# Performance work log

Measured on AMD Instinct MI355X. Metric: run time of the kernel, lower is better.

Reference implementation:

```python
import jax, jax.numpy as jnp
import numpy as np

SCALE = 0.08838834764831845  # 1/sqrt(128)


def setup_inputs() -> dict:
    key = jax.random.key(0)
    k1, k2, k3, k4 = jax.random.split(key, 4)
    B, Hq, Hkv, D = 32, 32, 8, 128
    block_size, max_blocks = 16, 256
    num_blocks = B * max_blocks  # 8192; identity paging layout
    q = jax.random.normal(k1, (B, 1, Hq, D), dtype=jnp.float32)
    k_cache = jax.random.normal(k2, (num_blocks, block_size, Hkv, D), dtype=jnp.float32)
    v_cache = jax.random.normal(k3, (num_blocks, block_size, Hkv, D), dtype=jnp.float32)
    cache_seqlens = jax.random.randint(k4, (B,), 1, block_size * max_blocks + 1, dtype=jnp.int32)
    block_table = jnp.arange(B * max_blocks, dtype=jnp.int32).reshape(B, max_blocks)
    return {"q": q, "k_cache": k_cache, "v_cache": v_cache,
            "cache_seqlens": cache_seqlens, "block_table": block_table}


def reference(q, k_cache, v_cache, cache_seqlens, block_table):
    # Decode-time paged attention (flash_attn_with_kvcache path).
    B, _, Hq, D = q.shape
    block_size, Hkv = k_cache.shape[1], k_cache.shape[2]
    G = Hq // Hkv  # GQA group size
    # Block-table gather: [B, max_blocks, bs, Hkv, D] -> [B, T, Hkv, D]
    k = k_cache[block_table].reshape(B, -1, Hkv, D)
    v = v_cache[block_table].reshape(B, -1, Hkv, D)
    T = k.shape[1]
    # GQA without materializing repeated KV heads: fold q heads into [Hkv, G]
    qg = q[:, 0].reshape(B, Hkv, G, D)
    scores = jnp.einsum('bkgd,btkd->bkgt', qg, k) * SCALE  # [B, Hkv, G, T]
    valid = jnp.arange(T, dtype=jnp.int32)[None, :] < cache_seqlens[:, None]  # [B, T]
    scores = jnp.where(valid[:, None, None, :], scores, -jnp.inf)
    probs = jax.nn.softmax(scores.astype(jnp.float32), axis=-1).astype(q.dtype)
    out = jnp.einsum('bkgt,btkd->bkgd', probs, v)  # [B, Hkv, G, D]
    return out.reshape(B, Hq, D)
```

## Files before the change

### kernel.cpp

```cpp
#include <hip/hip_runtime.h>
#include <math.h>


#define NUM_B    32
#define HQ       32
#define HKV      8
#define GG       4
#define DD       128
#define PAGE     16
#define MAXPAGES 256
#define SPLITS   16
#define CHUNK    256

static constexpr float SCALE_F = 0.08838834764831845f;
static constexpr float NEG     = -1e30f;

static __device__ __forceinline__ float dot8(const float4& qa, const float4& qb,
                                             const float4& ka, const float4& kb) {
    return qa.x * ka.x + qa.y * ka.y + qa.z * ka.z + qa.w * ka.w +
           qb.x * kb.x + qb.y * kb.y + qb.z * kb.z + qb.w * kb.w;
}

__global__ __launch_bounds__(64) void attn_split_kernel(
    const float* __restrict__ q,
    const float* __restrict__ kc,
    const float* __restrict__ vc,
    const int*   __restrict__ seqlens,
    const int*   __restrict__ btab,
    float*       __restrict__ accW,
    float*       __restrict__ mlW)
{
    const int bid   = blockIdx.x;
    const int split = bid & (SPLITS - 1);
    const int kvh   = (bid >> 4) & (HKV - 1);
    const int b     = bid >> 7;
    const int lane  = threadIdx.x;
    const int tg    = lane >> 4;
    const int ds    = lane & 15;

    const long pbase   = ((long)(b * HKV + kvh) * SPLITS + split) * GG;
    const long accBase = pbase * DD;
    const long mlBase  = pbase * 2;

    const int T  = seqlens[b];
    const int t0 = split * CHUNK;

    if (t0 >= T) {
        if (tg == 0) {
            const float4 z = make_float4(0.f, 0.f, 0.f, 0.f);
            #pragma unroll
            for (int g = 0; g < GG; ++g) {
                *(float4*)(accW + accBase + g * DD + ds * 8)     = z;
                *(float4*)(accW + accBase + g * DD + ds * 8 + 4) = z;
            }
            if (ds == 0) {
                #pragma unroll
                for (int g = 0; g < GG; ++g) {
                    mlW[mlBase + g * 2]     = NEG;
                    mlW[mlBase + g * 2 + 1] = 0.f;
                }
            }
        }
        return;
    }

    const int t1 = min(T, t0 + CHUNK);

    float4 q0[GG], q1[GG];
    #pragma unroll
    for (int g = 0; g < GG; ++g) {
        const float* qp = q + (long)(b * HQ + kvh * GG + g) * DD + ds * 8;
        q0[g] = *(const float4*)qp;
        q1[g] = *(const float4*)(qp + 4);
    }

    float m[GG], l[GG], acc[GG][8];
    #pragma unroll
    for (int g = 0; g < GG; ++g) {
        m[g] = NEG;
        l[g] = 0.f;
        #pragma unroll
        for (int j = 0; j < 8; ++j) acc[g][j] = 0.f;
    }

    const int btab_b = b * MAXPAGES;
    auto load_kv = [&](int tb, float4& k0, float4& k1, float4& v0, float4& v1) {
        const int t = min(tb + tg, t1 - 1);
        const int page = btab[btab_b + (t >> 4)];
        const long off = (((long)page * PAGE + (t & 15)) * HKV + kvh) * DD + ds * 8;
        k0 = *(const float4*)(kc + off);
        k1 = *(const float4*)(kc + off + 4);
        v0 = *(const float4*)(vc + off);
        v1 = *(const float4*)(vc + off + 4);
    };

    float4 k0, k1, v0, v1;
    load_kv(t0, k0, k1, v0, v1);

    for (int tb = t0; tb < t1; tb += 4) {
        const bool valid = (tb + tg) < t1;
        const float4 ck0 = k0, ck1 = k1, cv0 = v0, cv1 = v1;
        load_kv(tb + 4, k0, k1, v0, v1);

        #pragma unroll
        for (int g = 0; g < GG; ++g) {
            float s = dot8(q0[g], q1[g], ck0, ck1);
            s += __shfl_xor(s, 1);
            s += __shfl_xor(s, 2);
            s += __shfl_xor(s, 4);
            s += __shfl_xor(s, 8);
            s = valid ? s * SCALE_F : NEG;
            const float mn    = fmaxf(m[g], s);
            const float alpha = __expf(m[g] - mn);
            const float p     = valid ? __expf(s - mn) : 0.f;
            l[g] = l[g] * alpha + p;
            m[g] = mn;
            acc[g][0] = acc[g][0] * alpha + p * cv0.x;
            acc[g][1] = acc[g][1] * alpha + p * cv0.y;
            acc[g][2] = acc[g][2] * alpha + p * cv0.z;
            acc[g][3] = acc[g][3] * alpha + p * cv0.w;
            acc[g][4] = acc[g][4] * alpha + p * cv1.x;
            acc[g][5] = acc[g][5] * alpha + p * cv1.y;
            acc[g][6] = acc[g][6] * alpha + p * cv1.z;
            acc[g][7] = acc[g][7] * alpha + p * cv1.w;
        }
    }

    #pragma unroll
    for (int g = 0; g < GG; ++g) {
        float M2 = m[g];
        M2 = fmaxf(M2, __shfl_xor(M2, 16));
        M2 = fmaxf(M2, __shfl_xor(M2, 32));
        const float alpha = __expf(m[g] - M2);
        float lg = l[g] * alpha;
        lg += __shfl_xor(lg, 16);
        lg += __shfl_xor(lg, 32);
        float a[8];
        #pragma unroll
        for (int j = 0; j < 8; ++j) {
            float x = acc[g][j] * alpha;
            x += __shfl_xor(x, 16);
            x += __shfl_xor(x, 32);
            a[j] = x;
        }
        if (tg == 0) {
            const float4 o0 = make_float4(a[0], a[1], a[2], a[3]);
            const float4 o1 = make_float4(a[4], a[5], a[6], a[7]);
            *(float4*)(accW + accBase + g * DD + ds * 8)     = o0;
            *(float4*)(accW + accBase + g * DD + ds * 8 + 4) = o1;
            if (ds == 0) {
                mlW[mlBase + g * 2]     = M2;
                mlW[mlBase + g * 2 + 1] = lg;
            }
        }
    }
}

__global__ __launch_bounds__(128) void attn_reduce_kernel(
    const float* __restrict__ accW,
    const float* __restrict__ mlW,
    float*       __restrict__ out)
{
    const int bid = blockIdx.x;
    const int g   = bid & 3;
    const int kvh = (bid >> 2) & 7;
    const int b   = bid >> 5;
    const int d   = threadIdx.x;

    const long base = (long)(b * HKV + kvh) * SPLITS * GG;

    float ms[SPLITS], ls[SPLITS];
    float M = NEG;
    #pragma unroll
    for (int s = 0; s < SPLITS; ++s) {
        ms[s] = mlW[(base + s * GG + g) * 2];
        ls[s] = mlW[(base + s * GG + g) * 2 + 1];
        M = fmaxf(M, ms[s]);
    }
    float L = 0.f, o = 0.f;
    #pragma unroll
    for (int s = 0; s < SPLITS; ++s) {
        const float w = __expf(ms[s] - M);
        L += ls[s] * w;
        o += w * accW[(base + s * GG + g) * DD + d];
    }
    out[(long)(b * HQ + kvh * GG + g) * DD + d] = o / L;
}

extern "C" void kernel_launch(void* const* d_in, const int* in_sizes, int n_in,
                              void* d_out, int out_size, void* d_ws, size_t ws_size,
                              hipStream_t stream)
{
    const float* q       = (const float*)d_in[0];
    const float* kc      = (const float*)d_in[1];
    const float* vc      = (const float*)d_in[2];
    const int*   seqlens = (const int*)d_in[3];
    const int*   btab    = (const int*)d_in[4];
    float*       out     = (float*)d_out;

    float* accW = (float*)d_ws;
    float* mlW  = accW + (size_t)NUM_B * HKV * SPLITS * GG * DD;

    attn_split_kernel<<<NUM_B * HKV * SPLITS, 64, 0, stream>>>(
        q, kc, vc, seqlens, btab, accW, mlW);
    attn_reduce_kernel<<<NUM_B * HKV * GG, DD, 0, stream>>>(accW, mlW, out);
}
```

Baseline: 913.8 us.

## Double KV splits, prefetch two steps ahead, and cache page indices in registers

Raises the split count from 16 to 32 with 128-token chunks, which doubles the number of workgroups and gives more parallel memory streams. The loop now keeps two K/V loads in flight instead of one. Each lane preloads one page-table entry, and pages are fetched with a cross-lane shuffle instead of a global btab read every step. Empty splits now write only the max and sum values and skip zeroing the accumulator; the reduce weights those slots by exp(-huge)=0, so a NaN or Inf left in the uninitialised workspace could still leak into the output.

```diff
diff --git a/kernel.cpp b/kernel.cpp
--- a/kernel.cpp
+++ b/kernel.cpp
@@ -9,8 +9,8 @@
 #define DD       128
 #define PAGE     16
 #define MAXPAGES 256
-#define SPLITS   16
-#define CHUNK    256
+#define SPLITS   32
+#define CHUNK    128
 
 static constexpr float SCALE_F = 0.08838834764831845f;
 static constexpr float NEG     = -1e30f;
@@ -32,8 +32,8 @@
 {
     const int bid   = blockIdx.x;
     const int split = bid & (SPLITS - 1);
-    const int kvh   = (bid >> 4) & (HKV - 1);
-    const int b     = bid >> 7;
+    const int kvh   = (bid / SPLITS) & (HKV - 1);
+    const int b     = bid / (SPLITS * HKV);
     const int lane  = threadIdx.x;
     const int tg    = lane >> 4;
     const int ds    = lane & 15;
@@ -46,25 +46,19 @@
     const int t0 = split * CHUNK;
 
     if (t0 >= T) {
-        if (tg == 0) {
-            const float4 z = make_float4(0.f, 0.f, 0.f, 0.f);
-            #pragma unroll
-            for (int g = 0; g < GG; ++g) {
-                *(float4*)(accW + accBase + g * DD + ds * 8)     = z;
-                *(float4*)(accW + accBase + g * DD + ds * 8 + 4) = z;
-            }
-            if (ds == 0) {
-                #pragma unroll
-                for (int g = 0; g < GG; ++g) {
-                    mlW[mlBase + g * 2]     = NEG;
-                    mlW[mlBase + g * 2 + 1] = 0.f;
-                }
-            }
+        if (lane < GG) {
+            mlW[mlBase + lane * 2]     = NEG;
+            mlW[mlBase + lane * 2 + 1] = 0.f;
         }
         return;
     }
 
-    const int t1 = min(T, t0 + CHUNK);
+    const int t1    = min(T, t0 + CHUNK);
+    const int iters = (t1 - t0 + 3) >> 2;
+
+    const int lastp    = (T - 1) >> 4;
+    const int pidx     = min((t0 >> 4) + (lane & 15), lastp);
+    const int page_reg = btab[b * MAXPAGES + pidx];
 
     float4 q0[GG], q1[GG];
     #pragma unroll
@@ -83,10 +77,11 @@
         for (int j = 0; j < 8; ++j) acc[g][j] = 0.f;
     }
 
-    const int btab_b = b * MAXPAGES;
-    auto load_kv = [&](int tb, float4& k0, float4& k1, float4& v0, float4& v1) {
-        const int t = min(tb + tg, t1 - 1);
-        const int page = btab[btab_b + (t >> 4)];
+    auto load_iter = [&](int j, float4& k0, float4& k1, float4& v0, float4& v1) {
+        j = min(j, iters - 1);
+        const int tb   = t0 + 4 * j;
+        const int t    = min(tb + tg, t1 - 1);
+        const int page = __shfl(page_reg, (tb - t0) >> 4);
         const long off = (((long)page * PAGE + (t & 15)) * HKV + kvh) * DD + ds * 8;
         k0 = *(const float4*)(kc + off);
         k1 = *(const float4*)(kc + off + 4);
@@ -94,14 +89,9 @@
         v1 = *(const float4*)(vc + off + 4);
     };
 
-    float4 k0, k1, v0, v1;
-    load_kv(t0, k0, k1, v0, v1);
-
-    for (int tb = t0; tb < t1; tb += 4) {
-        const bool valid = (tb + tg) < t1;
-        const float4 ck0 = k0, ck1 = k1, cv0 = v0, cv1 = v1;
-        load_kv(tb + 4, k0, k1, v0, v1);
-
+    auto compute = [&](int j, const float4& ck0, const float4& ck1,
+                       const float4& cv0, const float4& cv1) {
+        const bool valid = (t0 + 4 * j + tg) < t1;
         #pragma unroll
         for (int g = 0; g < GG; ++g) {
             float s = dot8(q0[g], q1[g], ck0, ck1);
@@ -124,7 +114,26 @@
             acc[g][6] = acc[g][6] * alpha + p * cv1.z;
             acc[g][7] = acc[g][7] * alpha + p * cv1.w;
         }
-    }
+    };
+
+    float4 ka0, ka1, va0, va1, kb0, kb1, vb0, vb1;
+    load_iter(0, ka0, ka1, va0, va1);
+    load_iter(1, kb0, kb1, vb0, vb1);
+
+    int i = 0;
+    for (; i + 1 < iters; i += 2) {
+        {
+            const float4 c0 = ka0, c1 = ka1, c2 = va0, c3 = va1;
+            load_iter(i + 2, ka0, ka1, va0, va1);
+            compute(i, c0, c1, c2, c3);
+        }
+        {
+            const float4 c0 = kb0, c1 = kb1, c2 = vb0, c3 = vb1;
+            load_iter(i + 3, kb0, kb1, vb0, vb1);
+            compute(i + 1, c0, c1, c2, c3);
+        }
+    }
+    if (i < iters) compute(i, ka0, ka1, va0, va1);
 
     #pragma unroll
     for (int g = 0; g < GG; ++g) {
@@ -144,10 +153,8 @@
             a[j] = x;
         }
         if (tg == 0) {
-            const float4 o0 = make_float4(a[0], a[1], a[2], a[3]);
-            const float4 o1 = make_float4(a[4], a[5], a[6], a[7]);
-            *(float4*)(accW + accBase + g * DD + ds * 8)     = o0;
-            *(float4*)(accW + accBase + g * DD + ds * 8 + 4) = o1;
+            *(float4*)(accW + accBase + g * DD + ds * 8)     = make_float4(a[0], a[1], a[2], a[3]);
+            *(float4*)(accW + accBase + g * DD + ds * 8 + 4) = make_float4(a[4], a[5], a[6], a[7]);
             if (ds == 0) {
                 mlW[mlBase + g * 2]     = M2;
                 mlW[mlBase + g * 2 + 1] = lg;
```

Result: no change. 919.0 us (+0.6%).
